# Optimization experiments

Hardware: AMD Instinct MI355X
Metric: run time of the kernel (lower is better)

The kernel has to match this reference:

```python
import jax, jax.numpy as jnp
import numpy as np

N_CELLS = 4096          # rows of sparse x
N_INPUT_GENES = 20000   # cols of sparse x == len(input_gene_list)
N_PRETRAINED = 30000    # rows of embedding table
NUM_HID = 128
NNZ = 2097152           # ~512 expressed genes per cell


def setup_inputs() -> dict:
    key = jax.random.key(0)
    k_val, k_row, k_col, k_gidx, k_emb = jax.random.split(key, 5)
    x_values = jax.random.uniform(k_val, (NNZ,), dtype=jnp.float32)
    x_rows = jnp.sort(jax.random.randint(k_row, (NNZ,), 0, N_CELLS))
    x_cols = jax.random.randint(k_col, (NNZ,), 0, N_INPUT_GENES)
    gene_idx = jax.random.randint(k_gidx, (N_INPUT_GENES,), 0, N_PRETRAINED)
    # nn.Parameter(torch.randn(...) * 0.005)
    embs = jax.random.normal(k_emb, (N_PRETRAINED, NUM_HID), dtype=jnp.float32) * 0.005
    return {"x_values": x_values, "x_rows": x_rows, "x_cols": x_cols,
            "gene_idx": gene_idx, "embs": embs}


def reference(x_values, x_rows, x_cols, gene_idx, embs):
    # feat = F.embedding(gene_idx, embs)           -> [G_in, H]
    # out  = torch.sparse.mm(x, feat)              -> [N_cells, H]
    # Fused: gather per-nnz embedding rows, scale by value, segment-sum by cell.
    feat = embs[gene_idx]                                   # [G_in, H]
    contrib = x_values[:, None] * feat[x_cols]              # [NNZ, H]
    out = jax.ops.segment_sum(contrib, x_rows,
                              num_segments=N_CELLS,
                              indices_are_sorted=True)      # [N_cells, H]
    return out
```

## Files before the change

kernel.cpp:

```cpp
#include <hip/hip_runtime.h>

#define NNZ_TOT    2097152
#define N_CELLS    4096
#define N_GIN      20000
#define N_PRE      30000
#define NUM_HID    128

#define GA_OFF    0
#define GA_BYTES  ((size_t)NNZ_TOT * 4)
#define E8_OFF    (GA_OFF + GA_BYTES)
#define E8_BYTES  ((size_t)N_PRE * NUM_HID)
#define RP_OFF    (E8_OFF + E8_BYTES)
#define RP_BYTES  ((((size_t)(N_CELLS + 1) * 4) + 255) & ~(size_t)255)
#define SC_OFF    (RP_OFF + RP_BYTES)
#define SC_BYTES  256
#define WS_NEED   (SC_OFF + SC_BYTES)

#define NB_GA ((NNZ_TOT + 255) / 256)
#define NB_RP ((N_CELLS + 256) / 256)
#define NB_MX 512

__global__ __launch_bounds__(256) void precompute_kernel(
    const int* __restrict__ xc, const int* __restrict__ gidx,
    const int* __restrict__ xr, const float* __restrict__ embs,
    int* __restrict__ g_arr, int* __restrict__ rp,
    unsigned int* __restrict__ sc)
{
    const int b = blockIdx.x;
    if (b < NB_GA) {
        const int i = b * 256 + threadIdx.x;
        if (i < NNZ_TOT) g_arr[i] = gidx[xc[i]];
    } else if (b < NB_GA + NB_RP) {
        const int r = (b - NB_GA) * 256 + threadIdx.x;
        if (r <= N_CELLS) {
            int lo = 0, hi = NNZ_TOT;
            while (lo < hi) {
                const int mid = (lo + hi) >> 1;
                if (xr[mid] < r) lo = mid + 1; else hi = mid;
            }
            rp[r] = lo;
        }
    } else {
        const int t = (b - NB_GA - NB_RP) * 256 + (int)threadIdx.x;
        const float4* __restrict__ e4 = reinterpret_cast<const float4*>(embs);
        float m = 0.f;
        for (int j = t; j < N_PRE * NUM_HID / 4; j += NB_MX * 256) {
            const float4 f = e4[j];
            m = fmaxf(m, fmaxf(fmaxf(fabsf(f.x), fabsf(f.y)),
                               fmaxf(fabsf(f.z), fabsf(f.w))));
        }
        for (int d = 1; d < 64; d <<= 1) m = fmaxf(m, __shfl_xor(m, d));
        if ((threadIdx.x & 63) == 0) atomicMax(sc, __float_as_uint(m));
    }
}

__global__ __launch_bounds__(256) void convert_embs8_kernel(
    const float* __restrict__ embs, const unsigned int* __restrict__ sc,
    unsigned int* __restrict__ e8)
{
    const int i = blockIdx.x * blockDim.x + threadIdx.x;
    const long idx = (long)i * 4;
    if (idx < (long)N_PRE * NUM_HID) {
        const float maxabs = __uint_as_float(*sc);
        const float s = (maxabs > 0.f) ? 127.0f / maxabs : 0.f;
        const float4 f = *reinterpret_cast<const float4*>(&embs[idx]);
        int b0 = (int)rintf(f.x * s) + 128;
        int b1 = (int)rintf(f.y * s) + 128;
        int b2 = (int)rintf(f.z * s) + 128;
        int b3 = (int)rintf(f.w * s) + 128;
        b0 = min(max(b0, 0), 255); b1 = min(max(b1, 0), 255);
        b2 = min(max(b2, 0), 255); b3 = min(max(b3, 0), 255);
        e8[i] = (unsigned)b0 | ((unsigned)b1 << 8) |
                ((unsigned)b2 << 16) | ((unsigned)b3 << 24);
    }
}

#define U2F0(w) ((float)((w) & 0xffu))
#define U2F1(w) ((float)(((w) >> 8)  & 0xffu))
#define U2F2(w) ((float)(((w) >> 16) & 0xffu))
#define U2F3(w) ((float)(((w) >> 24) & 0xffu))

__device__ __forceinline__ void fma16i(uint4 f, float vv,
                                       float4& a0, float4& a1,
                                       float4& a2, float4& a3, float& S) {
    a0.x = fmaf(vv, U2F0(f.x), a0.x);
    a0.y = fmaf(vv, U2F1(f.x), a0.y);
    a0.z = fmaf(vv, U2F2(f.x), a0.z);
    a0.w = fmaf(vv, U2F3(f.x), a0.w);
    a1.x = fmaf(vv, U2F0(f.y), a1.x);
    a1.y = fmaf(vv, U2F1(f.y), a1.y);
    a1.z = fmaf(vv, U2F2(f.y), a1.z);
    a1.w = fmaf(vv, U2F3(f.y), a1.w);
    a2.x = fmaf(vv, U2F0(f.z), a2.x);
    a2.y = fmaf(vv, U2F1(f.z), a2.y);
    a2.z = fmaf(vv, U2F2(f.z), a2.z);
    a2.w = fmaf(vv, U2F3(f.z), a2.w);
    a3.x = fmaf(vv, U2F0(f.w), a3.x);
    a3.y = fmaf(vv, U2F1(f.w), a3.y);
    a3.z = fmaf(vv, U2F2(f.w), a3.z);
    a3.w = fmaf(vv, U2F3(f.w), a3.w);
    S += vv;
}

__global__ __launch_bounds__(256) void omics_row8_kernel(
    const float*        __restrict__ xv,
    const int*          __restrict__ ga,
    const int*          __restrict__ rp,
    const unsigned int* __restrict__ e8,
    const unsigned int* __restrict__ sc,
    float*              __restrict__ out)
{
    const int wave = (blockIdx.x * blockDim.x + threadIdx.x) >> 6;
    const int lane = threadIdx.x & 63;
    const int sub  = lane & 7;
    const int oct  = lane >> 3;
    const int r    = __builtin_amdgcn_readfirstlane(wave);
    if (r >= N_CELLS) return;

    const uint4* __restrict__ ebq = reinterpret_cast<const uint4*>(e8);

    const int lo = rp[r];
    const int hi = rp[r + 1];

    float4 a0 = make_float4(0.f,0.f,0.f,0.f), a1 = a0, a2 = a0, a3 = a0;
    float4 b0 = a0, b1 = a0, b2 = a0, b3 = a0;
    float Sa = 0.f, Sb = 0.f;

    int i = lo;
    for (; i + 64 <= hi; i += 64) {
        const int i0 = i + oct;
        const int g0 = ga[i0];      const float v0 = xv[i0];
        const int g1 = ga[i0 + 8];  const float v1 = xv[i0 + 8];
        const int g2 = ga[i0 + 16]; const float v2 = xv[i0 + 16];
        const int g3 = ga[i0 + 24]; const float v3 = xv[i0 + 24];
        const int g4 = ga[i0 + 32]; const float v4 = xv[i0 + 32];
        const int g5 = ga[i0 + 40]; const float v5 = xv[i0 + 40];
        const int g6 = ga[i0 + 48]; const float v6 = xv[i0 + 48];
        const int g7 = ga[i0 + 56]; const float v7 = xv[i0 + 56];

        const uint4 f0 = ebq[(long)g0 * 8 + sub];
        const uint4 f1 = ebq[(long)g1 * 8 + sub];
        const uint4 f2 = ebq[(long)g2 * 8 + sub];
        const uint4 f3 = ebq[(long)g3 * 8 + sub];
        const uint4 f4 = ebq[(long)g4 * 8 + sub];
        const uint4 f5 = ebq[(long)g5 * 8 + sub];
        const uint4 f6 = ebq[(long)g6 * 8 + sub];
        const uint4 f7 = ebq[(long)g7 * 8 + sub];

        fma16i(f0, v0, a0, a1, a2, a3, Sa);
        fma16i(f1, v1, b0, b1, b2, b3, Sb);
        fma16i(f2, v2, a0, a1, a2, a3, Sa);
        fma16i(f3, v3, b0, b1, b2, b3, Sb);
        fma16i(f4, v4, a0, a1, a2, a3, Sa);
        fma16i(f5, v5, b0, b1, b2, b3, Sb);
        fma16i(f6, v6, a0, a1, a2, a3, Sa);
        fma16i(f7, v7, b0, b1, b2, b3, Sb);
    }
    for (; i < hi; i += 8) {
        const int  idx = i + oct;
        const bool ok  = idx < hi;
        const int   gg = ga[ok ? idx : lo];
        const float vv = ok ? xv[idx] : 0.f;
        const uint4 f  = ebq[(long)gg * 8 + sub];
        fma16i(f, vv, a0, a1, a2, a3, Sa);
    }

    a0.x += b0.x; a0.y += b0.y; a0.z += b0.z; a0.w += b0.w;
    a1.x += b1.x; a1.y += b1.y; a1.z += b1.z; a1.w += b1.w;
    a2.x += b2.x; a2.y += b2.y; a2.z += b2.z; a2.w += b2.w;
    a3.x += b3.x; a3.y += b3.y; a3.z += b3.z; a3.w += b3.w;
    Sa += Sb;

    #define RED(c) c += __shfl_xor(c, 8); c += __shfl_xor(c, 16); c += __shfl_xor(c, 32)
    RED(a0.x); RED(a0.y); RED(a0.z); RED(a0.w);
    RED(a1.x); RED(a1.y); RED(a1.z); RED(a1.w);
    RED(a2.x); RED(a2.y); RED(a2.z); RED(a2.w);
    RED(a3.x); RED(a3.y); RED(a3.z); RED(a3.w);
    RED(Sa);
    #undef RED

    if (oct == 0) {
        const float maxabs = __uint_as_float(*sc);
        const float sdec   = (maxabs > 0.f) ? maxabs / 127.0f : 0.f;
        const float c      = 128.0f * Sa;
        float* o = &out[(long)r * NUM_HID + sub * 16];
        *reinterpret_cast<float4*>(o)      = make_float4(
            sdec*(a0.x-c), sdec*(a0.y-c), sdec*(a0.z-c), sdec*(a0.w-c));
        *reinterpret_cast<float4*>(o + 4)  = make_float4(
            sdec*(a1.x-c), sdec*(a1.y-c), sdec*(a1.z-c), sdec*(a1.w-c));
        *reinterpret_cast<float4*>(o + 8)  = make_float4(
            sdec*(a2.x-c), sdec*(a2.y-c), sdec*(a2.z-c), sdec*(a2.w-c));
        *reinterpret_cast<float4*>(o + 12) = make_float4(
            sdec*(a3.x-c), sdec*(a3.y-c), sdec*(a3.z-c), sdec*(a3.w-c));
    }
}

__global__ __launch_bounds__(256) void omics_fp32_row_kernel(
    const float* __restrict__ xv, const int* __restrict__ xr,
    const int* __restrict__ xc, const int* __restrict__ gidx,
    const float* __restrict__ embs, float* __restrict__ out)
{
    const int wave = (blockIdx.x * blockDim.x + threadIdx.x) >> 6;
    const int lane = threadIdx.x & 63;
    if (wave >= N_CELLS) return;
    int lo = 0, hi = NNZ_TOT;
    while (lo < hi) { int m = (lo + hi) >> 1; if (xr[m] < wave) lo = m + 1; else hi = m; }
    int lo2 = lo, hi2 = NNZ_TOT;
    while (lo2 < hi2) { int m = (lo2 + hi2) >> 1; if (xr[m] < wave + 1) lo2 = m + 1; else hi2 = m; }
    const int h = lane * 2;
    float2 acc = make_float2(0.f, 0.f);
    for (int i = lo; i < lo2; ++i) {
        const float v = xv[i];
        const int   g = gidx[xc[i]];
        const float2 f = *reinterpret_cast<const float2*>(&embs[(long)g * NUM_HID + h]);
        acc.x = fmaf(v, f.x, acc.x);
        acc.y = fmaf(v, f.y, acc.y);
    }
    *reinterpret_cast<float2*>(&out[(long)wave * NUM_HID + h]) = acc;
}

extern "C" void kernel_launch(void* const* d_in, const int* in_sizes, int n_in,
                              void* d_out, int out_size, void* d_ws, size_t ws_size,
                              hipStream_t stream) {
    const float* xv   = (const float*)d_in[0];
    const int*   xr   = (const int*)  d_in[1];
    const int*   xc   = (const int*)  d_in[2];
    const int*   gidx = (const int*)  d_in[3];
    const float* embs = (const float*)d_in[4];
    float*       out  = (float*)d_out;

    if (ws_size >= WS_NEED) {
        int*          ga = (int*)((char*)d_ws + GA_OFF);
        unsigned int* e8 = (unsigned int*)((char*)d_ws + E8_OFF);
        int*          rp = (int*)((char*)d_ws + RP_OFF);
        unsigned int* sc = (unsigned int*)((char*)d_ws + SC_OFF);

        (void)hipMemsetAsync(sc, 0, 4, stream);

        precompute_kernel<<<NB_GA + NB_RP + NB_MX, 256, 0, stream>>>(
            xc, gidx, xr, embs, ga, rp, sc);
        convert_embs8_kernel<<<(N_PRE * NUM_HID / 4 + 255) / 256, 256, 0, stream>>>(
            embs, sc, e8);

        omics_row8_kernel<<<(N_CELLS * 64) / 256, 256, 0, stream>>>(
            xv, ga, rp, e8, sc, out);
    } else {
        omics_fp32_row_kernel<<<(N_CELLS * 64) / 256, 256, 0, stream>>>(
            xv, xr, xc, gidx, embs, out);
    }
}
```

Measured before the change: 141.9 us.

## Use per-row int8 scales, 16-bit gene indices, and drop global max pass

Replaces the single global max-abs int8 quantization with a per-embedding-row scale computed inside the conversion kernel. This removes the memset, the global max-reduction blocks and their atomic, and the serial dependency between finding the max and converting. The gathered gene index array is narrowed to 16-bit to halve its write and read traffic. In exchange, the main loop does an extra scalar gather of the row scale per nonzero, and byte-wise stores in the conversion kernel may be less efficient than packed word stores.

```diff
diff --git a/kernel.cpp b/kernel.cpp
--- a/kernel.cpp
+++ b/kernel.cpp
@@ -7,30 +7,28 @@
 #define NUM_HID    128
 
 #define GA_OFF    0
-#define GA_BYTES  ((size_t)NNZ_TOT * 4)
+#define GA_BYTES  ((((size_t)NNZ_TOT * 2) + 255) & ~(size_t)255)
 #define E8_OFF    (GA_OFF + GA_BYTES)
 #define E8_BYTES  ((size_t)N_PRE * NUM_HID)
-#define RP_OFF    (E8_OFF + E8_BYTES)
+#define RS_OFF    (E8_OFF + E8_BYTES)
+#define RS_BYTES  ((((size_t)N_PRE * 4) + 255) & ~(size_t)255)
+#define RP_OFF    (RS_OFF + RS_BYTES)
 #define RP_BYTES  ((((size_t)(N_CELLS + 1) * 4) + 255) & ~(size_t)255)
-#define SC_OFF    (RP_OFF + RP_BYTES)
-#define SC_BYTES  256
-#define WS_NEED   (SC_OFF + SC_BYTES)
+#define WS_NEED   (RP_OFF + RP_BYTES)
 
 #define NB_GA ((NNZ_TOT + 255) / 256)
 #define NB_RP ((N_CELLS + 256) / 256)
-#define NB_MX 512
 
 __global__ __launch_bounds__(256) void precompute_kernel(
     const int* __restrict__ xc, const int* __restrict__ gidx,
-    const int* __restrict__ xr, const float* __restrict__ embs,
-    int* __restrict__ g_arr, int* __restrict__ rp,
-    unsigned int* __restrict__ sc)
+    const int* __restrict__ xr, unsigned short* __restrict__ ga,
+    int* __restrict__ rp)
 {
     const int b = blockIdx.x;
     if (b < NB_GA) {
         const int i = b * 256 + threadIdx.x;
-        if (i < NNZ_TOT) g_arr[i] = gidx[xc[i]];
-    } else if (b < NB_GA + NB_RP) {
+        if (i < NNZ_TOT) ga[i] = (unsigned short)gidx[xc[i]];
+    } else {
         const int r = (b - NB_GA) * 256 + threadIdx.x;
         if (r <= N_CELLS) {
             int lo = 0, hi = NNZ_TOT;
@@ -40,39 +38,29 @@
             }
             rp[r] = lo;
         }
-    } else {
-        const int t = (b - NB_GA - NB_RP) * 256 + (int)threadIdx.x;
-        const float4* __restrict__ e4 = reinterpret_cast<const float4*>(embs);
-        float m = 0.f;
-        for (int j = t; j < N_PRE * NUM_HID / 4; j += NB_MX * 256) {
-            const float4 f = e4[j];
-            m = fmaxf(m, fmaxf(fmaxf(fabsf(f.x), fabsf(f.y)),
-                               fmaxf(fabsf(f.z), fabsf(f.w))));
-        }
-        for (int d = 1; d < 64; d <<= 1) m = fmaxf(m, __shfl_xor(m, d));
-        if ((threadIdx.x & 63) == 0) atomicMax(sc, __float_as_uint(m));
     }
 }
 
 __global__ __launch_bounds__(256) void convert_embs8_kernel(
-    const float* __restrict__ embs, const unsigned int* __restrict__ sc,
-    unsigned int* __restrict__ e8)
-{
-    const int i = blockIdx.x * blockDim.x + threadIdx.x;
-    const long idx = (long)i * 4;
-    if (idx < (long)N_PRE * NUM_HID) {
-        const float maxabs = __uint_as_float(*sc);
-        const float s = (maxabs > 0.f) ? 127.0f / maxabs : 0.f;
-        const float4 f = *reinterpret_cast<const float4*>(&embs[idx]);
-        int b0 = (int)rintf(f.x * s) + 128;
-        int b1 = (int)rintf(f.y * s) + 128;
-        int b2 = (int)rintf(f.z * s) + 128;
-        int b3 = (int)rintf(f.w * s) + 128;
-        b0 = min(max(b0, 0), 255); b1 = min(max(b1, 0), 255);
-        b2 = min(max(b2, 0), 255); b3 = min(max(b3, 0), 255);
-        e8[i] = (unsigned)b0 | ((unsigned)b1 << 8) |
-                ((unsigned)b2 << 16) | ((unsigned)b3 << 24);
-    }
+    const float* __restrict__ embs, unsigned char* __restrict__ e8,
+    float* __restrict__ rs)
+{
+    const int row  = (blockIdx.x * blockDim.x + threadIdx.x) >> 6;
+    const int lane = threadIdx.x & 63;
+    if (row >= N_PRE) return;
+    const long base = (long)row * NUM_HID;
+    const float e0 = embs[base + lane];
+    const float e1 = embs[base + 64 + lane];
+    float m = fmaxf(fabsf(e0), fabsf(e1));
+    for (int d = 1; d < 64; d <<= 1) m = fmaxf(m, __shfl_xor(m, d));
+    const float sinv = (m > 0.f) ? 127.0f / m : 0.f;
+    int b0 = (int)rintf(e0 * sinv) + 128;
+    int b1 = (int)rintf(e1 * sinv) + 128;
+    b0 = min(max(b0, 0), 255);
+    b1 = min(max(b1, 0), 255);
+    e8[base + lane]      = (unsigned char)b0;
+    e8[base + 64 + lane] = (unsigned char)b1;
+    if (lane == 0) rs[row] = m * (1.0f / 127.0f);
 }
 
 #define U2F0(w) ((float)((w) & 0xffu))
@@ -103,12 +91,12 @@
 }
 
 __global__ __launch_bounds__(256) void omics_row8_kernel(
-    const float*        __restrict__ xv,
-    const int*          __restrict__ ga,
-    const int*          __restrict__ rp,
-    const unsigned int* __restrict__ e8,
-    const unsigned int* __restrict__ sc,
-    float*              __restrict__ out)
+    const float*          __restrict__ xv,
+    const unsigned short* __restrict__ ga,
+    const int*            __restrict__ rp,
+    const unsigned int*   __restrict__ e8,
+    const float*          __restrict__ rs,
+    float*                __restrict__ out)
 {
     const int wave = (blockIdx.x * blockDim.x + threadIdx.x) >> 6;
     const int lane = threadIdx.x & 63;
@@ -129,14 +117,14 @@
     int i = lo;
     for (; i + 64 <= hi; i += 64) {
         const int i0 = i + oct;
-        const int g0 = ga[i0];      const float v0 = xv[i0];
-        const int g1 = ga[i0 + 8];  const float v1 = xv[i0 + 8];
-        const int g2 = ga[i0 + 16]; const float v2 = xv[i0 + 16];
-        const int g3 = ga[i0 + 24]; const float v3 = xv[i0 + 24];
-        const int g4 = ga[i0 + 32]; const float v4 = xv[i0 + 32];
-        const int g5 = ga[i0 + 40]; const float v5 = xv[i0 + 40];
-        const int g6 = ga[i0 + 48]; const float v6 = xv[i0 + 48];
-        const int g7 = ga[i0 + 56]; const float v7 = xv[i0 + 56];
+        const int g0 = ga[i0];      const float w0 = xv[i0]      * rs[g0];
+        const int g1 = ga[i0 + 8];  const float w1 = xv[i0 + 8]  * rs[g1];
+        const int g2 = ga[i0 + 16]; const float w2 = xv[i0 + 16] * rs[g2];
+        const int g3 = ga[i0 + 24]; const float w3 = xv[i0 + 24] * rs[g3];
+        const int g4 = ga[i0 + 32]; const float w4 = xv[i0 + 32] * rs[g4];
+        const int g5 = ga[i0 + 40]; const float w5 = xv[i0 + 40] * rs[g5];
+        const int g6 = ga[i0 + 48]; const float w6 = xv[i0 + 48] * rs[g6];
+        const int g7 = ga[i0 + 56]; const float w7 = xv[i0 + 56] * rs[g7];
 
         const uint4 f0 = ebq[(long)g0 * 8 + sub];
         const uint4 f1 = ebq[(long)g1 * 8 + sub];
@@ -147,20 +135,20 @@
         const uint4 f6 = ebq[(long)g6 * 8 + sub];
         const uint4 f7 = ebq[(long)g7 * 8 + sub];
 
-        fma16i(f0, v0, a0, a1, a2, a3, Sa);
-        fma16i(f1, v1, b0, b1, b2, b3, Sb);
-        fma16i(f2, v2, a0, a1, a2, a3, Sa);
-        fma16i(f3, v3, b0, b1, b2, b3, Sb);
-        fma16i(f4, v4, a0, a1, a2, a3, Sa);
-        fma16i(f5, v5, b0, b1, b2, b3, Sb);
-        fma16i(f6, v6, a0, a1, a2, a3, Sa);
-        fma16i(f7, v7, b0, b1, b2, b3, Sb);
+        fma16i(f0, w0, a0, a1, a2, a3, Sa);
+        fma16i(f1, w1, b0, b1, b2, b3, Sb);
+        fma16i(f2, w2, a0, a1, a2, a3, Sa);
+        fma16i(f3, w3, b0, b1, b2, b3, Sb);
+        fma16i(f4, w4, a0, a1, a2, a3, Sa);
+        fma16i(f5, w5, b0, b1, b2, b3, Sb);
+        fma16i(f6, w6, a0, a1, a2, a3, Sa);
+        fma16i(f7, w7, b0, b1, b2, b3, Sb);
     }
     for (; i < hi; i += 8) {
         const int  idx = i + oct;
         const bool ok  = idx < hi;
         const int   gg = ga[ok ? idx : lo];
-        const float vv = ok ? xv[idx] : 0.f;
+        const float vv = ok ? xv[idx] * rs[gg] : 0.f;
         const uint4 f  = ebq[(long)gg * 8 + sub];
         fma16i(f, vv, a0, a1, a2, a3, Sa);
     }
@@ -180,18 +168,12 @@
     #undef RED
 
     if (oct == 0) {
-        const float maxabs = __uint_as_float(*sc);
-        const float sdec   = (maxabs > 0.f) ? maxabs / 127.0f : 0.f;
-        const float c      = 128.0f * Sa;
+        const float c = 128.0f * Sa;
         float* o = &out[(long)r * NUM_HID + sub * 16];
-        *reinterpret_cast<float4*>(o)      = make_float4(
-            sdec*(a0.x-c), sdec*(a0.y-c), sdec*(a0.z-c), sdec*(a0.w-c));
-        *reinterpret_cast<float4*>(o + 4)  = make_float4(
-            sdec*(a1.x-c), sdec*(a1.y-c), sdec*(a1.z-c), sdec*(a1.w-c));
-        *reinterpret_cast<float4*>(o + 8)  = make_float4(
-            sdec*(a2.x-c), sdec*(a2.y-c), sdec*(a2.z-c), sdec*(a2.w-c));
-        *reinterpret_cast<float4*>(o + 12) = make_float4(
-            sdec*(a3.x-c), sdec*(a3.y-c), sdec*(a3.z-c), sdec*(a3.w-c));
+        *reinterpret_cast<float4*>(o)      = make_float4(a0.x-c, a0.y-c, a0.z-c, a0.w-c);
+        *reinterpret_cast<float4*>(o + 4)  = make_float4(a1.x-c, a1.y-c, a1.z-c, a1.w-c);
+        *reinterpret_cast<float4*>(o + 8)  = make_float4(a2.x-c, a2.y-c, a2.z-c, a2.w-c);
+        *reinterpret_cast<float4*>(o + 12) = make_float4(a3.x-c, a3.y-c, a3.z-c, a3.w-c);
     }
 }
 
@@ -230,20 +212,17 @@
     float*       out  = (float*)d_out;
 
     if (ws_size >= WS_NEED) {
-        int*          ga = (int*)((char*)d_ws + GA_OFF);
-        unsigned int* e8 = (unsigned int*)((char*)d_ws + E8_OFF);
-        int*          rp = (int*)((char*)d_ws + RP_OFF);
-        unsigned int* sc = (unsigned int*)((char*)d_ws + SC_OFF);
-
-        (void)hipMemsetAsync(sc, 0, 4, stream);
-
-        precompute_kernel<<<NB_GA + NB_RP + NB_MX, 256, 0, stream>>>(
-            xc, gidx, xr, embs, ga, rp, sc);
-        convert_embs8_kernel<<<(N_PRE * NUM_HID / 4 + 255) / 256, 256, 0, stream>>>(
-            embs, sc, e8);
+        unsigned short* ga = (unsigned short*)((char*)d_ws + GA_OFF);
+        unsigned char*  e8 = (unsigned char*)((char*)d_ws + E8_OFF);
+        float*          rs = (float*)((char*)d_ws + RS_OFF);
+        int*            rp = (int*)((char*)d_ws + RP_OFF);
+
+        precompute_kernel<<<NB_GA + NB_RP, 256, 0, stream>>>(xc, gidx, xr, ga, rp);
+        convert_embs8_kernel<<<(N_PRE * 64 + 255) / 256, 256, 0, stream>>>(
+            embs, e8, rs);
 
         omics_row8_kernel<<<(N_CELLS * 64) / 256, 256, 0, stream>>>(
-            xv, ga, rp, e8, sc, out);
+            xv, ga, rp, (const unsigned int*)e8, rs, out);
     } else {
         omics_fp32_row_kernel<<<(N_CELLS * 64) / 256, 256, 0, stream>>>(
             xv, xr, xc, gidx, embs, out);
```

New measurement: 123.4 us. 13.0% less time.
